# Optimization experiments

Hardware: AMD Instinct MI355X
Metric: run time of the kernel (lower is better)

The kernel has to match this reference:

```python
import jax, jax.numpy as jnp
import numpy as np

EPS = 1e-5
K = 16
DILATION = 1

def _bn(x, g, b, axes):
    # BatchNorm in training mode: batch statistics over all axes except channel (last)
    m = jnp.mean(x, axis=axes, keepdims=True)
    v = jnp.var(x, axis=axes, keepdims=True)
    return (x - m) * jax.lax.rsqrt(v + EPS) * g + b

def _knn_idx(p, q, k):
    # p: [B,N,3], q: [B,M,3] -> indices [B,M,k] of nearest points in p for each q
    d = (jnp.sum(q * q, -1)[:, :, None]
         - 2.0 * jnp.einsum('bmc,bnc->bmn', q, p)
         + jnp.sum(p * p, -1)[:, None, :])  # [B,M,N]
    _, idx = jax.lax.top_k(-d, k)
    return jax.lax.stop_gradient(idx)

def setup_inputs() -> dict:
    key = jax.random.key(0)
    ks = jax.random.split(key, 16)
    B, N, M, Cin, Cout = 8, 8192, 2048, 64, 128
    mid, K2 = Cout // 4, K * K
    s = 0.02
    d = {
        'p': jax.random.normal(ks[0], (B, N, 3), jnp.float32),
        'q': jax.random.normal(ks[1], (B, M, 3), jnp.float32),
        'x': jax.random.normal(ks[2], (B, Cin, N), jnp.float32),
        # mlp: two 1x1 convs (3->mid->mid) each with BN
        'W1': jax.random.normal(ks[3], (mid, 3), jnp.float32) * s,
        'b1': jnp.zeros((mid,), jnp.float32),
        'g1': jnp.ones((mid,), jnp.float32), 'be1': jnp.zeros((mid,), jnp.float32),
        'W2': jax.random.normal(ks[4], (mid, mid), jnp.float32) * s,
        'b2': jnp.zeros((mid,), jnp.float32),
        'g2': jnp.ones((mid,), jnp.float32), 'be2': jnp.zeros((mid,), jnp.float32),
        # stn: conv [1,K] (3->K^2), then two 1x1 convs (K^2->K^2)
        'Ws1': jax.random.normal(ks[5], (K2, 3, K), jnp.float32) * s,
        'bs1': jnp.zeros((K2,), jnp.float32),
        'gs1': jnp.ones((K2,), jnp.float32), 'bes1': jnp.zeros((K2,), jnp.float32),
        'Ws2': jax.random.normal(ks[6], (K2, K2), jnp.float32) * s,
        'bs2': jnp.zeros((K2,), jnp.float32),
        'gs2': jnp.ones((K2,), jnp.float32), 'bes2': jnp.zeros((K2,), jnp.float32),
        'Ws3': jax.random.normal(ks[7], (K2, K2), jnp.float32) * s,
        'bs3': jnp.zeros((K2,), jnp.float32),
        # final conv [1,K]: (Cin+mid -> Cout) with BN
        'Wc': jax.random.normal(ks[8], (Cout, Cin + mid, K), jnp.float32) * s,
        'bc': jnp.zeros((Cout,), jnp.float32),
        'gc': jnp.ones((Cout,), jnp.float32), 'bec': jnp.zeros((Cout,), jnp.float32),
    }
    return d

def reference(p, q, x, W1, b1, g1, be1, W2, b2, g2, be2,
              Ws1, bs1, gs1, bes1, Ws2, bs2, gs2, bes2, Ws3, bs3,
              Wc, bc, gc, bec):
    B, M = q.shape[0], q.shape[1]
    idx = _knn_idx(p, q, K * DILATION)[..., ::DILATION]  # [B,M,K]
    # gather neighbor coords and center: p_hat [B,M,K,3]
    p_n = jax.vmap(lambda a, i: a[i])(p, idx)
    p_hat = p_n - q[:, :, None, :]
    # mlp (pointwise convs, channel-last)
    h = jax.nn.relu(_bn(jnp.einsum('bmkc,oc->bmko', p_hat, W1) + b1, g1, be1, (0, 1, 2)))
    h = jax.nn.relu(_bn(jnp.einsum('bmkc,oc->bmko', h, W2) + b2, g2, be2, (0, 1, 2)))
    # gather features: x [B,Cin,N] -> [B,M,K,Cin]
    xt = jnp.transpose(x, (0, 2, 1))
    x_n = jax.vmap(lambda a, i: a[i])(xt, idx)
    x_hat = jnp.concatenate([h, x_n], axis=-1)  # [B,M,K,mid+Cin]
    # stn -> transform T [B,M,K,K]
    t = jax.nn.relu(_bn(jnp.einsum('bmkc,ock->bmo', p_hat, Ws1) + bs1, gs1, bes1, (0, 1)))
    t = jax.nn.relu(_bn(jnp.einsum('bmi,oi->bmo', t, Ws2) + bs2, gs2, bes2, (0, 1)))
    t = jnp.einsum('bmi,oi->bmo', t, Ws3) + bs3  # [B,M,K*K]
    T = t.reshape(B, M, K, K)
    x2 = jnp.einsum('bmij,bmjc->bmic', T, x_hat)  # [B,M,K,mid+Cin]
    out = jax.nn.relu(_bn(jnp.einsum('bmkc,ock->bmo', x2, Wc) + bc, gc, bec, (0, 1)))  # [B,M,Cout]
    return (q, jnp.transpose(out, (0, 2, 1)))  # q, x:[B,Cout,M]
```

## Files before the change

kernel.cpp:

```cpp
#include <hip/hip_runtime.h>
#include <hip/hip_bf16.h>


#define EPS 1e-5f

constexpr int Bb   = 8;
constexpr int Np   = 8192;
constexpr int Mq   = 2048;
constexpr int COUT = 128;
constexpr int BM   = Bb * Mq;
constexpr int BMK  = BM * 16;
constexpr int GC   = 16;
constexpr int NC   = GC * GC * GC;
constexpr int CAP  = 320;

typedef __attribute__((ext_vector_type(8))) short short8;
typedef __attribute__((ext_vector_type(4))) short short4v;
typedef __attribute__((ext_vector_type(4))) float f32x4;

__device__ __forceinline__ unsigned short f2bf(float x) {
  unsigned u = __float_as_uint(x);
  u += 0x7fffu + ((u >> 16) & 1u);
  return (unsigned short)(u >> 16);
}
__device__ __forceinline__ float bf2f_lo(unsigned v) { return __uint_as_float(v << 16); }
__device__ __forceinline__ float bf2f_hi(unsigned v) { return __uint_as_float(v & 0xffff0000u); }
__device__ __forceinline__ float bfround(float x) {
  return __uint_as_float(((unsigned)f2bf(x)) << 16);
}

__device__ __forceinline__ int cell_of(float c) {
  int v = (int)floorf(c * 2.0f + 8.0f);
  return v < 0 ? 0 : (v > 15 ? 15 : v);
}

__device__ __forceinline__ unsigned enc_dist(float d) {
  unsigned uu = __float_as_uint(d);
  return uu ^ (((unsigned)(((int)uu) >> 31)) | 0x80000000u);
}

__device__ __forceinline__ void bsort64(unsigned long long& v, int lane) {
#pragma unroll
  for (int k = 2; k <= 64; k <<= 1) {
#pragma unroll
    for (int jj = k >> 1; jj > 0; jj >>= 1) {
      unsigned long long o = __shfl_xor(v, jj);
      bool keepMin = (((lane & k) == 0) == ((lane & jj) == 0));
      unsigned long long mn = v < o ? v : o;
      unsigned long long mx = v < o ? o : v;
      v = keepMin ? mn : mx;
    }
  }
}
__device__ __forceinline__ void bmerge64(unsigned long long& v, int lane) {
#pragma unroll
  for (int jj = 32; jj > 0; jj >>= 1) {
    unsigned long long o = __shfl_xor(v, jj);
    bool keepMin = ((lane & jj) == 0);
    unsigned long long mn = v < o ? v : o;
    unsigned long long mx = v < o ? o : v;
    v = keepMin ? mn : mx;
  }
}
__device__ __forceinline__ unsigned long long sort_smallest64(const unsigned long long* buf,
                                                              int C, int lane) {
  unsigned long long run = (lane < C) ? buf[lane] : ~0ULL;
  bsort64(run, lane);
  for (int b2 = 64; b2 < C; b2 += 64) {
    unsigned long long v = (b2 + lane < C) ? buf[b2 + lane] : ~0ULL;
    bsort64(v, lane);
    unsigned long long vr = __shfl_xor(v, 63);
    unsigned long long m = run < vr ? run : vr;
    bmerge64(m, lane);
    run = m;
  }
  return run;
}


__device__ __forceinline__ void bn1_compute(int o, const float* __restrict__ st,
                                            const float* __restrict__ W1,
                                            const float* __restrict__ b1,
                                            const float* __restrict__ g1,
                                            const float* __restrict__ be1,
                                            float* sc_out, float* shf_out) {
  float n = (float)BMK;
  float w0 = W1[3 * o], w1 = W1[3 * o + 1], w2 = W1[3 * o + 2], b = b1[o];
  float s0 = st[0], s1 = st[1], s2 = st[2];
  float m00 = st[3], m11 = st[4], m22 = st[5], m01 = st[6], m02 = st[7], m12 = st[8];
  float ws = (w0 * s0 + w1 * s1 + w2 * s2) / n;
  float mean = b + ws;
  float quad = w0 * w0 * m00 + w1 * w1 * m11 + w2 * w2 * m22 +
               2.f * (w0 * w1 * m01 + w0 * w2 * m02 + w1 * w2 * m12);
  float ex2 = quad / n + 2.f * b * ws + b * b;
  float var = ex2 - mean * mean;
  float sc = g1[o] * rsqrtf(var + EPS);
  *sc_out = sc;
  *shf_out = be1[o] - mean * sc + b * sc;
}

__global__ __launch_bounds__(256) void prep_kernel(const float* __restrict__ p,
                                                   const float* __restrict__ x,
                                                   const float* __restrict__ Wc,
                                                   const float* __restrict__ Ws1,
                                                   float4* __restrict__ pp4,
                                                   float* __restrict__ xt,
                                                   unsigned short* __restrict__ wcrp,
                                                   unsigned short* __restrict__ ws1r,
                                                   int* __restrict__ hist) {
  __shared__ float tile[64][65];
  int blk = blockIdx.x;
  int tid = threadIdx.x;
  if (blk < 256) {
    int i = blk * 256 + tid;
    float px = p[3 * i], py = p[3 * i + 1], pz = p[3 * i + 2];
    float pp = __fadd_rn(__fadd_rn(__fmul_rn(px, px), __fmul_rn(py, py)), __fmul_rn(pz, pz));
    pp4[i] = make_float4(px, py, pz, pp);
    int b = i >> 13;
    int cid = (cell_of(px) << 8) | (cell_of(py) << 4) | cell_of(pz);
    atomicAdd(&hist[b * NC + cid], 1);
  } else if (blk < 1280) {
    int bx = blk - 256;
    int b = bx >> 7;
    int n0 = (bx & 127) << 6;
    int nl = tid & 63;
    int r0 = tid >> 6;
    const float* xb = x + (size_t)b * 64 * Np;
    for (int c = r0; c < 64; c += 4) tile[c][nl] = xb[(size_t)c * Np + n0 + nl];
    __syncthreads();
    float* xtb = xt + (size_t)b * Np * 64;
    for (int n = r0; n < 64; n += 4) xtb[(size_t)(n0 + n) * 64 + nl] = tile[nl][n];
  } else if (blk < 2048) {
    int g = (blk - 1280) * 256 + tid;
    if (g < 128 * 1536) {
      int o = g / 1536, r = g % 1536;
      int c = r % 96, j = r / 96;
      wcrp[g] = f2bf(Wc[(size_t)o * 1536 + c * 16 + j]);
    }
  } else {
    int g = (blk - 2048) * 256 + tid;
    int o = g >> 6, i = g & 63;
    float val = 0.f;
    if (i < 48) {
      int k = i / 3, c = i - 3 * k;
      val = Ws1[(size_t)o * 48 + c * 16 + k];
    }
    unsigned short h = f2bf(val);
    float hf = __uint_as_float(((unsigned)h) << 16);
    unsigned short l = f2bf(val - hf);
    ws1r[g] = h;
    ws1r[16384 + g] = l;
  }
}

__global__ __launch_bounds__(256) void prefix_kernel(const int* __restrict__ hist,
                                                     int* __restrict__ cellstart,
                                                     int* __restrict__ cursor) {
  __shared__ int ls[256];
  int b = blockIdx.x, t = threadIdx.x;
  const int* h = hist + b * NC;
  int loc[16], s = 0;
#pragma unroll
  for (int k = 0; k < 16; ++k) { loc[k] = h[t * 16 + k]; s += loc[k]; }
  ls[t] = s;
  __syncthreads();
  for (int off = 1; off < 256; off <<= 1) {
    int v = (t >= off) ? ls[t - off] : 0;
    __syncthreads();
    ls[t] += v;
    __syncthreads();
  }
  int run = ls[t] - s;
  int* cs = cellstart + b * (NC + 1);
  int* cu = cursor + b * NC;
#pragma unroll
  for (int k = 0; k < 16; ++k) {
    cs[t * 16 + k] = run;
    cu[t * 16 + k] = run;
    run += loc[k];
  }
  if (t == 255) cs[NC] = run;
}

__global__ __launch_bounds__(256) void scatter_kernel(const float4* __restrict__ pp4,
                                                      int* __restrict__ cursor,
                                                      float4* __restrict__ sp4,
                                                      int* __restrict__ sidx) {
  int i = blockIdx.x * 256 + threadIdx.x;
  int b = i >> 13;
  float4 pv = pp4[i];
  int cid = (cell_of(pv.x) << 8) | (cell_of(pv.y) << 4) | cell_of(pv.z);
  int pos = atomicAdd(&cursor[b * NC + cid], 1);
  sp4[(size_t)b * Np + pos] = pv;
  sidx[(size_t)b * Np + pos] = i & 8191;
}

__global__ __launch_bounds__(256) void knn_kernel(const float4* __restrict__ pp4,
                                                  const float4* __restrict__ sp4,
                                                  const int* __restrict__ sidx,
                                                  const int* __restrict__ cellstart,
                                                  const float* __restrict__ q,
                                                  int* __restrict__ idx_out) {
  __shared__ unsigned long long cand[4][CAP];
  int tid = threadIdx.x;
  int wslot = tid >> 6;
  int qi = blockIdx.x * 4 + wslot;
  int lane = tid & 63;
  int b = qi >> 11;
  const float4* pb = pp4 + (size_t)b * Np;
  const float4* sp = sp4 + (size_t)b * Np;
  const int* sx = sidx + (size_t)b * Np;
  const int* cs = cellstart + b * (NC + 1);
  const float* qp = q + (size_t)qi * 3;
  float qx = qp[0], qy = qp[1], qz = qp[2];
  float qqv = __fadd_rn(__fadd_rn(__fmul_rn(qx, qx), __fmul_rn(qy, qy)), __fmul_rn(qz, qz));
  float tau_f = INFINITY;

  {
    int cx = cell_of(qx), cy = cell_of(qy), cz = cell_of(qz);
    int alo = 0, blo = 0, nbw = 1, ncols = 1, zlo = 0, zhi = 0;
    int myS = 0, myE = 0;
    for (int r = 0;; ++r) {
      alo = cx - r; if (alo < 0) alo = 0;
      int ahi = cx + r; if (ahi > 15) ahi = 15;
      blo = cy - r; if (blo < 0) blo = 0;
      int bhi = cy + r; if (bhi > 15) bhi = 15;
      zlo = cz - r; if (zlo < 0) zlo = 0;
      zhi = cz + r; if (zhi > 15) zhi = 15;
      nbw = bhi - blo + 1;
      ncols = (ahi - alo + 1) * nbw;
      int total = 0;
      for (int l0 = 0; l0 < ncols; l0 += 64) {
        int l = l0 + lane;
        int sL = 0, eL = 0;
        if (l < ncols) {
          int da = l / nbw, db = l - da * nbw;
          int cbase = ((alo + da) << 8) | ((blo + db) << 4);
          sL = cs[cbase + zlo];
          eL = cs[cbase + zhi + 1];
        }
        if (l0 == 0) { myS = sL; myE = eL; }
        total += eL - sL;
      }
#pragma unroll
      for (int o = 32; o > 0; o >>= 1) total += __shfl_xor(total, o);
      if (total >= 16 || r >= 15) break;
    }
    unsigned u0 = 0xFFFFFFFFu, u1 = 0xFFFFFFFFu;
    int wcnt = 0;
    int ccen = (cx - alo) * nbw + (cy - blo);
    for (int c2 = 0; c2 < ncols && wcnt < 128; ++c2) {
      int cc = (c2 == 0) ? ccen : (c2 <= ccen ? c2 - 1 : c2);
      int s0, e;
      if (cc < 64) {
        s0 = __shfl(myS, cc);
        e = __shfl(myE, cc);
      } else {
        int da = cc / nbw, db = cc - da * nbw;
        int cbase = ((alo + da) << 8) | ((blo + db) << 4);
        s0 = cs[cbase + zlo];
        e = cs[cbase + zhi + 1];
      }
      for (int off = s0; off < e && wcnt < 128; off += 64) {
        int rem = e - off; if (rem > 64) rem = 64;
        int rot = wcnt & 63;
        int rel = (lane - rot) & 63;
        int g = wcnt + rel;
        if (rel < rem && g < 128) {
          float4 pv = sp[off + rel];
          float ee = __fmaf_rn(qz, pv.z, __fmaf_rn(qy, pv.y, __fmul_rn(qx, pv.x)));
          float d = __fadd_rn(__fsub_rn(qqv, __fmul_rn(2.0f, ee)), pv.w);
          unsigned uu = enc_dist(d);
          if (g < 64) u0 = uu; else u1 = uu;
        }
        wcnt += rem;
      }
    }
    unsigned lo = 0u, hi = 0xFF800000u;
    for (int it = 0; it < 20; ++it) {
      unsigned mid = lo + ((hi - lo) >> 1);
      int c = (int)__popcll(__ballot(u0 <= mid)) + (int)__popcll(__ballot(u1 <= mid));
      if (c >= 16) hi = mid; else lo = mid + 1;
    }
    tau_f = (hi >= 0x80000000u) ? __uint_as_float(hi ^ 0x80000000u)
                                : __uint_as_float(~hi);
  }

  int cnt = 0;
  unsigned long long lanebelow = (1ULL << lane) - 1ULL;
  {
    float R = sqrtf(fmaxf(tau_f, 0.f) + 3e-5f) * 1.0005f;
    int ax0 = cell_of(qx - R), ax1 = cell_of(qx + R);
    int ay0 = cell_of(qy - R), ay1 = cell_of(qy + R);
    int az0 = cell_of(qz - R), az1 = cell_of(qz + R);
    int nby = ay1 - ay0 + 1;
    int ncols = (ax1 - ax0 + 1) * nby;
    int myS = 0, myE = 0;
    if (lane < ncols) {
      int da = lane / nby, db = lane - da * nby;
      int cbase = ((ax0 + da) << 8) | ((ay0 + db) << 4);
      myS = cs[cbase + az0];
      myE = cs[cbase + az1 + 1];
    }
    for (int cc = 0; cc < ncols; ++cc) {
      int s0, e;
      if (cc < 64) {
        s0 = __shfl(myS, cc);
        e = __shfl(myE, cc);
      } else {
        int da = cc / nby, db = cc - da * nby;
        int cbase = ((ax0 + da) << 8) | ((ay0 + db) << 4);
        s0 = cs[cbase + az0];
        e = cs[cbase + az1 + 1];
      }
      for (int off = s0; off < e; off += 64) {
        int pos = off + lane;
        bool valid = pos < e;
        float4 pv = sp[valid ? pos : s0];
        float ee = __fmaf_rn(qz, pv.z, __fmaf_rn(qy, pv.y, __fmul_rn(qx, pv.x)));
        float d = __fadd_rn(__fsub_rn(qqv, __fmul_rn(2.0f, ee)), pv.w);
        if (!valid) d = __uint_as_float(0x7FC00000u);
        unsigned long long mask = __ballot(d <= tau_f);
        if (mask) {
          if (d <= tau_f) {
            int oi = sx[pos];
            unsigned uu = enc_dist(d);
            int wp = cnt + (int)__popcll(mask & lanebelow);
            if (wp < CAP)
              cand[wslot][wp] = (((unsigned long long)uu) << 32) | (unsigned)oi;
          }
          cnt += (int)__popcll(mask);
        }
      }
    }
  }
  __syncthreads();

  if (cnt <= CAP) {
    unsigned long long run = sort_smallest64(&cand[wslot][0], cnt, lane);
    if (lane < 16)
      idx_out[(size_t)qi * 16 + lane] = (int)(run & 0xffffffffULL);
  } else {
    unsigned long long kk = ~0ULL;
    float tl = tau_f;
    for (int base = 0; base < Np; base += 64) {
      float4 pv = pb[base + lane];
      float ee = __fmaf_rn(qz, pv.z, __fmaf_rn(qy, pv.y, __fmul_rn(qx, pv.x)));
      float dv = __fadd_rn(__fsub_rn(qqv, __fmul_rn(2.0f, ee)), pv.w);
      unsigned long long mask = __ballot(dv <= tl);
      if (mask) {
        unsigned uu = enc_dist(dv);
        unsigned long long cd = (((unsigned long long)uu) << 32) | (unsigned)(base + lane);
        do {
          int src = __ffsll((unsigned long long)mask) - 1;
          mask &= mask - 1;
          unsigned long long ck = __shfl(cd, src);
          unsigned long long up = __shfl_up(kk, 1);
          if (lane == 0) up = 0ULL;
          if (lane < 16 && ck < kk) kk = (up > ck) ? up : ck;
        } while (mask);
        unsigned long long tt = __shfl(kk, 15);
        unsigned tm = (unsigned)(tt >> 32);
        unsigned inv2 = tm ^ ((tm & 0x80000000u) ? 0x80000000u : 0xFFFFFFFFu);
        float tc = (tm == 0xFFFFFFFFu) ? INFINITY : __uint_as_float(inv2);
        if (tc < tl) tl = tc;
      }
    }
    if (lane < 16)
      idx_out[(size_t)qi * 16 + lane] = (int)(kk & 0xffffffffULL);
  }
}

__global__ __launch_bounds__(256) void phat_stats_kernel(const float4* __restrict__ pp4,
                                                         const float* __restrict__ q,
                                                         const int* __restrict__ idx,
                                                         float* __restrict__ phat,
                                                         float* __restrict__ stats) {
  float a[9];
#pragma unroll
  for (int k = 0; k < 9; ++k) a[k] = 0.f;
  int tid = threadIdx.x;
  for (int it = 0; it < 4; ++it) {
    int bmk = blockIdx.x * 256 + tid + it * 65536;
    int bm = bmk >> 4;
    int b = bm >> 11;
    int j = idx[bmk];
    float4 pv = pp4[(size_t)b * Np + j];
    const float* qp = q + (size_t)bm * 3;
    float h0 = pv.x - qp[0], h1 = pv.y - qp[1], h2 = pv.z - qp[2];
    phat[(size_t)bmk * 3 + 0] = h0;
    phat[(size_t)bmk * 3 + 1] = h1;
    phat[(size_t)bmk * 3 + 2] = h2;
    a[0] += h0; a[1] += h1; a[2] += h2;
    a[3] += h0 * h0; a[4] += h1 * h1; a[5] += h2 * h2;
    a[6] += h0 * h1; a[7] += h0 * h2; a[8] += h1 * h2;
  }
#pragma unroll
  for (int off = 32; off > 0; off >>= 1)
#pragma unroll
    for (int k = 0; k < 9; ++k) a[k] += __shfl_down(a[k], off);
  __shared__ float ls[9];
  if (tid < 9) ls[tid] = 0.f;
  __syncthreads();
  if ((tid & 63) == 0)
    for (int k = 0; k < 9; ++k) atomicAdd(&ls[k], a[k]);
  __syncthreads();
  if (tid < 9) atomicAdd(&stats[tid], ls[tid]);
}

__global__ __launch_bounds__(256) void stats2_kernel(const float* __restrict__ phat,
                                                     const float* __restrict__ stats,
                                                     const float* __restrict__ W1,
                                                     const float* __restrict__ b1,
                                                     const float* __restrict__ g1,
                                                     const float* __restrict__ be1,
                                                     const float* __restrict__ W2,
                                                     const float* __restrict__ b2,
                                                     float* __restrict__ stats2) {
  __shared__ float hsh[256 * 36];
  __shared__ float w2s[32 * 33];
  __shared__ float w1s[96], sc1[32], sh1[32], b2s[32], ls[64];
  int tid = threadIdx.x;
  if (tid < 32) {
    bn1_compute(tid, stats, W1, b1, g1, be1, &sc1[tid], &sh1[tid]);
    b2s[tid] = b2[tid];
  }
  if (tid < 96) w1s[tid] = W1[tid];
  if (tid < 64) ls[tid] = 0.f;
  for (int e = tid; e < 1024; e += 256) w2s[(e >> 5) * 33 + (e & 31)] = W2[e];
  __syncthreads();
  {
    int bmk = blockIdx.x * 256 + tid;
    float h0 = phat[(size_t)bmk * 3], hy = phat[(size_t)bmk * 3 + 1], hz = phat[(size_t)bmk * 3 + 2];
#pragma unroll
    for (int o4 = 0; o4 < 8; ++o4) {
      float4 r;
      float* rp = (float*)&r;
#pragma unroll
      for (int u = 0; u < 4; ++u) {
        int o = o4 * 4 + u;
        float t = w1s[3 * o] * h0 + w1s[3 * o + 1] * hy + w1s[3 * o + 2] * hz;
        rp[u] = fmaxf(0.f, t * sc1[o] + sh1[o]);
      }
      *(float4*)&hsh[tid * 36 + o4 * 4] = r;
    }
  }
  __syncthreads();
  int oc = tid & 31, grp = tid >> 5;
  float wrow[32];
#pragma unroll
  for (int c = 0; c < 32; ++c) wrow[c] = w2s[oc * 33 + c];
  float bias = b2s[oc];
  float ss = 0.f, qq = 0.f;
  for (int r = 0; r < 32; ++r) {
    int row = grp * 32 + r;
    float a = bias;
    const float4* hr = (const float4*)&hsh[row * 36];
#pragma unroll
    for (int c4 = 0; c4 < 8; ++c4) {
      float4 hv = hr[c4];
      a += hv.x * wrow[c4 * 4 + 0];
      a += hv.y * wrow[c4 * 4 + 1];
      a += hv.z * wrow[c4 * 4 + 2];
      a += hv.w * wrow[c4 * 4 + 3];
    }
    ss += a;
    qq += a * a;
  }
  atomicAdd(&ls[oc], ss);
  atomicAdd(&ls[32 + oc], qq);
  __syncthreads();
  if (tid < 64) atomicAdd(&stats2[tid], ls[tid]);
}

__global__ __launch_bounds__(256) void stn1_kernel(const float* __restrict__ phat,
                                                   const unsigned short* __restrict__ ws1r,
                                                   const float* __restrict__ bs1,
                                                   float* __restrict__ pt1,
                                                   float* __restrict__ spt1) {
  __shared__ unsigned short Ah[64 * 72], Al[64 * 72], Bh[128 * 72], Bl[128 * 72];
  __shared__ float ls[256];
  int tid = threadIdx.x;
  ls[tid] = 0.f;
  int mb = blockIdx.x >> 1, nb = blockIdx.x & 1;
  int bm0 = mb * 64, o0 = nb * 128;
  {
    int zr = tid >> 2, zc = 48 + (tid & 3) * 4;
    *(unsigned long long*)&Ah[zr * 72 + zc] = 0ULL;
    *(unsigned long long*)&Al[zr * 72 + zc] = 0ULL;
  }
  {
    int ar = tid >> 2, aseg = tid & 3;
    const float* Ap = phat + (size_t)(bm0 + ar) * 48 + aseg * 12;
    float4 v0 = *(const float4*)(Ap);
    float4 v1 = *(const float4*)(Ap + 4);
    float4 v2 = *(const float4*)(Ap + 8);
    float av[12] = {v0.x, v0.y, v0.z, v0.w, v1.x, v1.y, v1.z, v1.w, v2.x, v2.y, v2.z, v2.w};
    unsigned long long ph[3] = {0ULL, 0ULL, 0ULL}, pl[3] = {0ULL, 0ULL, 0ULL};
#pragma unroll
    for (int t = 0; t < 12; ++t) {
      unsigned short h = f2bf(av[t]);
      float hf = __uint_as_float(((unsigned)h) << 16);
      unsigned short l = f2bf(av[t] - hf);
      ph[t >> 2] |= ((unsigned long long)h) << ((t & 3) * 16);
      pl[t >> 2] |= ((unsigned long long)l) << ((t & 3) * 16);
    }
    int base = ar * 72 + aseg * 12;
#pragma unroll
    for (int t4 = 0; t4 < 3; ++t4) {
      *(unsigned long long*)&Ah[base + t4 * 4] = ph[t4];
      *(unsigned long long*)&Al[base + t4 * 4] = pl[t4];
    }
  }
#pragma unroll
  for (int pass = 0; pass < 4; ++pass) {
    int g = pass * 2048 + tid * 8;
    int br = g >> 6, i2 = g & 63;
    short8 vh = *(const short8*)&ws1r[(size_t)(o0 + br) * 64 + i2];
    short8 vl = *(const short8*)&ws1r[16384 + (size_t)(o0 + br) * 64 + i2];
    *(short8*)&Bh[br * 72 + i2] = vh;
    *(short8*)&Bl[br * 72 + i2] = vl;
  }
  __syncthreads();
  int wid = tid >> 6, lane = tid & 63;
  int wm = wid >> 1, wn = wid & 1;
  int mh = lane & 15, quad = lane >> 4;
  f32x4 acc[2][4];
#pragma unroll
  for (int a = 0; a < 2; ++a)
#pragma unroll
    for (int bq = 0; bq < 4; ++bq) acc[a][bq] = (f32x4){0.f, 0.f, 0.f, 0.f};
#pragma unroll
  for (int kc = 0; kc < 2; ++kc) {
    int ko = kc * 32 + quad * 8;
#pragma unroll
    for (int mt = 0; mt < 2; ++mt) {
      short8 ah = *(const short8*)&Ah[(wm * 32 + mt * 16 + mh) * 72 + ko];
      short8 al = *(const short8*)&Al[(wm * 32 + mt * 16 + mh) * 72 + ko];
#pragma unroll
      for (int nt = 0; nt < 4; ++nt) {
        short8 bh = *(const short8*)&Bh[(wn * 64 + nt * 16 + mh) * 72 + ko];
        short8 bl = *(const short8*)&Bl[(wn * 64 + nt * 16 + mh) * 72 + ko];
        acc[mt][nt] = __builtin_amdgcn_mfma_f32_16x16x32_bf16(ah, bh, acc[mt][nt], 0, 0, 0);
        acc[mt][nt] = __builtin_amdgcn_mfma_f32_16x16x32_bf16(ah, bl, acc[mt][nt], 0, 0, 0);
        acc[mt][nt] = __builtin_amdgcn_mfma_f32_16x16x32_bf16(al, bh, acc[mt][nt], 0, 0, 0);
      }
    }
  }
#pragma unroll
  for (int mt = 0; mt < 2; ++mt)
#pragma unroll
    for (int nt = 0; nt < 4; ++nt) {
      int colL = wn * 64 + nt * 16 + mh;
      int col = o0 + colL;
      float bvv = bs1[col];
      float ps = 0.f, pq = 0.f;
#pragma unroll
      for (int r = 0; r < 4; ++r) {
        float val = acc[mt][nt][r] + bvv;
        pt1[(size_t)(bm0 + wm * 32 + mt * 16 + quad * 4 + r) * 256 + col] = val;
        ps += val;
        pq += val * val;
      }
      atomicAdd(&ls[colL], ps);
      atomicAdd(&ls[128 + colL], pq);
    }
  __syncthreads();
  if (tid < 128) {
    atomicAdd(&spt1[o0 + tid], ls[tid]);
    atomicAdd(&spt1[256 + o0 + tid], ls[128 + tid]);
  }
}

__global__ __launch_bounds__(256) void stn_mm_kernel(const float* __restrict__ in,
                                                     const float* __restrict__ sums,
                                                     const float* __restrict__ gg,
                                                     const float* __restrict__ be,
                                                     const float* __restrict__ W,
                                                     const float* __restrict__ bias,
                                                     float* __restrict__ out,
                                                     float* __restrict__ outstats,
                                                     int do_stats) {
  __shared__ unsigned short As[64 * 40], Bs[128 * 40];
  __shared__ float scA[256], shA[256], ls[256];
  int tid = threadIdx.x;
  ls[tid] = 0.f;
  {
    float n = (float)BM;
    float mean = sums[tid] / n;
    float var = sums[256 + tid] / n - mean * mean;
    float s = gg[tid] * rsqrtf(var + EPS);
    scA[tid] = s;
    shA[tid] = be[tid] - mean * s;
  }
  int mb = blockIdx.x >> 1, nb = blockIdx.x & 1;
  int bm0 = mb * 64, o0 = nb * 128;
  int wid = tid >> 6, lane = tid & 63;
  int wm = wid >> 1, wn = wid & 1;
  int mh = lane & 15, quad = lane >> 4;
  f32x4 acc[2][4];
#pragma unroll
  for (int a = 0; a < 2; ++a)
#pragma unroll
    for (int bq = 0; bq < 4; ++bq) acc[a][bq] = (f32x4){0.f, 0.f, 0.f, 0.f};
  int ar = tid >> 2, aseg = tid & 3;
  const float* Ag = in + (size_t)(bm0 + ar) * 256 + aseg * 8;
  int aoff = ar * 40 + aseg * 8;
  int ci = aseg * 8;
  for (int i0 = 0; i0 < 256; i0 += 32) {
    __syncthreads();
    float4 v0 = *(const float4*)(Ag + i0);
    float4 v1 = *(const float4*)(Ag + i0 + 4);
    float av[8] = {v0.x, v0.y, v0.z, v0.w, v1.x, v1.y, v1.z, v1.w};
    short8 ap;
#pragma unroll
    for (int k = 0; k < 8; ++k)
      ap[k] = (short)f2bf(fmaxf(0.f, av[k] * scA[i0 + ci + k] + shA[i0 + ci + k]));
    *(short8*)&As[aoff] = ap;
#pragma unroll
    for (int jb = 0; jb < 2; ++jb) {
      int br = jb * 64 + ar;
      const float* Bg = W + (size_t)(o0 + br) * 256 + aseg * 8;
      float4 u0 = *(const float4*)(Bg + i0);
      float4 u1 = *(const float4*)(Bg + i0 + 4);
      float bv[8] = {u0.x, u0.y, u0.z, u0.w, u1.x, u1.y, u1.z, u1.w};
      short8 bp;
#pragma unroll
      for (int k = 0; k < 8; ++k) bp[k] = (short)f2bf(bv[k]);
      *(short8*)&Bs[br * 40 + aseg * 8] = bp;
    }
    __syncthreads();
#pragma unroll
    for (int mt = 0; mt < 2; ++mt) {
      short8 af = *(const short8*)&As[(wm * 32 + mt * 16 + mh) * 40 + quad * 8];
#pragma unroll
      for (int nt = 0; nt < 4; ++nt) {
        short8 bf = *(const short8*)&Bs[(wn * 64 + nt * 16 + mh) * 40 + quad * 8];
        acc[mt][nt] = __builtin_amdgcn_mfma_f32_16x16x32_bf16(af, bf, acc[mt][nt], 0, 0, 0);
      }
    }
  }
#pragma unroll
  for (int mt = 0; mt < 2; ++mt)
#pragma unroll
    for (int nt = 0; nt < 4; ++nt) {
      int colL = wn * 64 + nt * 16 + mh;
      int col = o0 + colL;
      float bvv = bias[col];
      float ps = 0.f, pq = 0.f;
#pragma unroll
      for (int r = 0; r < 4; ++r) {
        float val = acc[mt][nt][r] + bvv;
        out[(size_t)(bm0 + wm * 32 + mt * 16 + quad * 4 + r) * 256 + col] = val;
        ps += val;
        pq += val * val;
      }
      if (do_stats) {
        atomicAdd(&ls[colL], ps);
        atomicAdd(&ls[128 + colL], pq);
      }
    }
  if (do_stats) {
    __syncthreads();
    if (tid < 128) {
      atomicAdd(&outstats[o0 + tid], ls[tid]);
      atomicAdd(&outstats[256 + o0 + tid], ls[128 + tid]);
    }
  }
}

__global__ __launch_bounds__(256) void xhat_x2_kernel(const float* __restrict__ phat,
                                                      const float* __restrict__ stats,
                                                      const float* __restrict__ stats2,
                                                      const float* __restrict__ W1,
                                                      const float* __restrict__ b1,
                                                      const float* __restrict__ g1,
                                                      const float* __restrict__ be1,
                                                      const float* __restrict__ W2,
                                                      const float* __restrict__ b2,
                                                      const float* __restrict__ g2,
                                                      const float* __restrict__ be2,
                                                      const float* __restrict__ xt,
                                                      const int* __restrict__ idx,
                                                      const float* __restrict__ Tbuf,
                                                      unsigned short* __restrict__ x2) {
  __shared__ unsigned xh[256 * 17];
  __shared__ float Tst[256 * 16];
  __shared__ float sc1[32], sh1[32], sc2[32], sh2[32];
  int tid = threadIdx.x;
  if (tid < 32) {
    bn1_compute(tid, stats, W1, b1, g1, be1, &sc1[tid], &sh1[tid]);
    float n = (float)BMK;
    float mean = stats2[tid] / n;
    float var = stats2[32 + tid] / n - mean * mean;
    float s = g2[tid] * rsqrtf(var + EPS);
    sc2[tid] = s;
    sh2[tid] = be2[tid] - mean * s + b2[tid] * s;
  }
  __syncthreads();
  int bm0 = blockIdx.x * 16;
  int b = bm0 >> 11;
  int bml = tid >> 4, j = tid & 15;
  int bmk = (bm0 + bml) * 16 + j;
  {
    float h0 = phat[(size_t)bmk * 3], hy = phat[(size_t)bmk * 3 + 1], hz = phat[(size_t)bmk * 3 + 2];
    float h1v[32];
#pragma unroll
    for (int o = 0; o < 32; ++o) {
      float t = W1[3 * o] * h0 + W1[3 * o + 1] * hy + W1[3 * o + 2] * hz;
      h1v[o] = fmaxf(0.f, t * sc1[o] + sh1[o]);
    }
#pragma unroll
    for (int o4 = 0; o4 < 8; ++o4) {
      float r[4];
#pragma unroll
      for (int u = 0; u < 4; ++u) {
        int o = o4 * 4 + u;
        float a = 0.f;
#pragma unroll
        for (int c = 0; c < 32; ++c) a += h1v[c] * W2[o * 32 + c];
        r[u] = fmaxf(0.f, a * sc2[o] + sh2[o]);
      }
      xh[tid * 17 + o4 * 2] = (unsigned)f2bf(r[0]) | (((unsigned)f2bf(r[1])) << 16);
      xh[tid * 17 + o4 * 2 + 1] = (unsigned)f2bf(r[2]) | (((unsigned)f2bf(r[3])) << 16);
    }
    const float4* tg = (const float4*)(Tbuf + (size_t)(bm0 + bml) * 256 + j * 16);
    float4* td = (float4*)&Tst[tid * 16];
    td[0] = tg[0]; td[1] = tg[1]; td[2] = tg[2]; td[3] = tg[3];
  }
  __syncthreads();
  int cl = j;
  {
    float vlo[16], vhi[16];
#pragma unroll
    for (int jj = 0; jj < 16; ++jj) {
      unsigned uv = xh[(bml * 16 + jj) * 17 + cl];
      vlo[jj] = bf2f_lo(uv);
      vhi[jj] = bf2f_hi(uv);
    }
    for (int jo = 0; jo < 16; ++jo) {
      const float4* tr4 = (const float4*)&Tst[(bml * 16 + jo) * 16];
      float4 ta = tr4[0], tb = tr4[1], tc = tr4[2], tdd = tr4[3];
      float trow[16] = {ta.x, ta.y, ta.z, ta.w, tb.x, tb.y, tb.z, tb.w,
                        tc.x, tc.y, tc.z, tc.w, tdd.x, tdd.y, tdd.z, tdd.w};
      float a0 = 0.f, a1 = 0.f;
#pragma unroll
      for (int jj = 0; jj < 16; ++jj) {
        a0 += trow[jj] * vlo[jj];
        a1 += trow[jj] * vhi[jj];
      }
      unsigned* dst = (unsigned*)(x2 + (size_t)((bm0 + bml) * 16 + jo) * 96);
      dst[cl] = (unsigned)f2bf(a0) | (((unsigned)f2bf(a1)) << 16);
    }
  }
  {
    const int* idxrow = idx + (size_t)(bm0 + bml) * 16;
    float v0[16], v1[16], v2[16], v3[16];
#pragma unroll
    for (int jj = 0; jj < 16; ++jj) {
      int jx = idxrow[jj];
      float4 xv = *(const float4*)(xt + ((size_t)b * Np + jx) * 64 + cl * 4);
      v0[jj] = bfround(xv.x);
      v1[jj] = bfround(xv.y);
      v2[jj] = bfround(xv.z);
      v3[jj] = bfround(xv.w);
    }
    for (int jo = 0; jo < 16; ++jo) {
      const float4* tr4 = (const float4*)&Tst[(bml * 16 + jo) * 16];
      float4 ta = tr4[0], tb = tr4[1], tc = tr4[2], tdd = tr4[3];
      float trow[16] = {ta.x, ta.y, ta.z, ta.w, tb.x, tb.y, tb.z, tb.w,
                        tc.x, tc.y, tc.z, tc.w, tdd.x, tdd.y, tdd.z, tdd.w};
      float a0 = 0.f, a1 = 0.f, a2 = 0.f, a3 = 0.f;
#pragma unroll
      for (int jj = 0; jj < 16; ++jj) {
        float t = trow[jj];
        a0 += t * v0[jj];
        a1 += t * v1[jj];
        a2 += t * v2[jj];
        a3 += t * v3[jj];
      }
      unsigned* dst = (unsigned*)(x2 + (size_t)((bm0 + bml) * 16 + jo) * 96);
      dst[16 + cl * 2] = (unsigned)f2bf(a0) | (((unsigned)f2bf(a1)) << 16);
      dst[17 + cl * 2] = (unsigned)f2bf(a2) | (((unsigned)f2bf(a3)) << 16);
    }
  }
}

__global__ __launch_bounds__(256) void preout_kernel(const unsigned short* __restrict__ x2,
                                                     const unsigned short* __restrict__ Wcrp,
                                                     const float* __restrict__ bc,
                                                     float* __restrict__ pout,
                                                     float* __restrict__ spout) {
  __shared__ unsigned short As[32 * 40], Bs[128 * 40];
  __shared__ float ls[256];
  int tid = threadIdx.x;
  ls[tid] = 0.f;
  int bm0 = blockIdx.x * 32;
  int wid = tid >> 6, lane = tid & 63;
  int mh = lane & 15, quad = lane >> 4;
  f32x4 acc[2][2];
#pragma unroll
  for (int a = 0; a < 2; ++a)
#pragma unroll
    for (int bq = 0; bq < 2; ++bq) acc[a][bq] = (f32x4){0.f, 0.f, 0.f, 0.f};
  int ar = tid >> 3, aseg = tid & 7;
  int br = tid >> 1, bseg = tid & 1;
  const unsigned short* Ag = x2 + (size_t)(bm0 + ar) * 1536 + aseg * 4;
  const unsigned short* Bg = Wcrp + (size_t)br * 1536 + bseg * 16;
  int aoff = ar * 40 + aseg * 4;
  int boff = br * 40 + bseg * 16;
  short4v a_pre = *(const short4v*)Ag;
  short8 b_pre0 = *(const short8*)Bg;
  short8 b_pre1 = *(const short8*)(Bg + 8);
  for (int i0 = 0; i0 < 1536; i0 += 32) {
    __syncthreads();
    *(short4v*)&As[aoff] = a_pre;
    *(short8*)&Bs[boff] = b_pre0;
    *(short8*)&Bs[boff + 8] = b_pre1;
    __syncthreads();
    if (i0 + 32 < 1536) {
      a_pre = *(const short4v*)(Ag + i0 + 32);
      b_pre0 = *(const short8*)(Bg + i0 + 32);
      b_pre1 = *(const short8*)(Bg + i0 + 40);
    }
#pragma unroll
    for (int mt = 0; mt < 2; ++mt) {
      short8 af = *(const short8*)&As[(mt * 16 + mh) * 40 + quad * 8];
#pragma unroll
      for (int nt = 0; nt < 2; ++nt) {
        short8 bf = *(const short8*)&Bs[(wid * 32 + nt * 16 + mh) * 40 + quad * 8];
        acc[mt][nt] = __builtin_amdgcn_mfma_f32_16x16x32_bf16(af, bf, acc[mt][nt], 0, 0, 0);
      }
    }
  }
#pragma unroll
  for (int mt = 0; mt < 2; ++mt)
#pragma unroll
    for (int nt = 0; nt < 2; ++nt) {
      int col = wid * 32 + nt * 16 + mh;
      float bvv = bc[col];
      float ps = 0.f, pq = 0.f;
#pragma unroll
      for (int r = 0; r < 4; ++r) {
        float val = acc[mt][nt][r] + bvv;
        pout[(size_t)(bm0 + mt * 16 + quad * 4 + r) * 128 + col] = val;
        ps += val;
        pq += val * val;
      }
      atomicAdd(&ls[col], ps);
      atomicAdd(&ls[128 + col], pq);
    }
  __syncthreads();
  atomicAdd(&spout[tid], ls[tid]);
}

__global__ __launch_bounds__(256) void final_kernel(const float* __restrict__ q,
                                                    const float* __restrict__ pout,
                                                    const float* __restrict__ scs,
                                                    const float* __restrict__ gc,
                                                    const float* __restrict__ bec,
                                                    float* __restrict__ dout) {
  __shared__ float ldsT[128 * 65];
  int blk = blockIdx.x;
  int tid = threadIdx.x;
  if (blk < 192) {
    int g = blk * 256 + tid;
    dout[g] = q[g];
    return;
  }
  int blk2 = blk - 192;
  int b = blk2 >> 5;
  int m0 = (blk2 & 31) * 64;
  int row = tid >> 2, seg = tid & 3;
  const float4* src = (const float4*)(pout + ((size_t)(b * Mq) + m0 + row) * 128 + seg * 32);
#pragma unroll
  for (int k4 = 0; k4 < 8; ++k4) {
    float4 v = src[k4];
    int o = seg * 32 + k4 * 4;
    ldsT[(o + 0) * 65 + row] = v.x;
    ldsT[(o + 1) * 65 + row] = v.y;
    ldsT[(o + 2) * 65 + row] = v.z;
    ldsT[(o + 3) * 65 + row] = v.w;
  }
  __syncthreads();
  int lane = tid & 63, wv = tid >> 6;
  float n = (float)BM;
  float* base = dout + (size_t)BM * 3 + (size_t)b * COUT * Mq + m0;
#pragma unroll
  for (int rep = 0; rep < 32; ++rep) {
    int o = wv * 32 + rep;
    float mean = scs[o] / n;
    float var = scs[128 + o] / n - mean * mean;
    float s = gc[o] * rsqrtf(var + EPS);
    float shv = bec[o] - mean * s;
    float v = ldsT[o * 65 + lane];
    base[(size_t)o * Mq + lane] = fmaxf(0.f, v * s + shv);
  }
}

extern "C" void kernel_launch(void* const* d_in, const int* in_sizes, int n_in, void* d_out,
                              int out_size, void* d_ws, size_t ws_size, hipStream_t stream) {
  const float* p = (const float*)d_in[0];
  const float* q = (const float*)d_in[1];
  const float* x = (const float*)d_in[2];
  const float* W1 = (const float*)d_in[3];
  const float* b1 = (const float*)d_in[4];
  const float* g1 = (const float*)d_in[5];
  const float* be1 = (const float*)d_in[6];
  const float* W2 = (const float*)d_in[7];
  const float* b2 = (const float*)d_in[8];
  const float* g2 = (const float*)d_in[9];
  const float* be2 = (const float*)d_in[10];
  const float* Ws1 = (const float*)d_in[11];
  const float* bs1 = (const float*)d_in[12];
  const float* gs1 = (const float*)d_in[13];
  const float* bes1 = (const float*)d_in[14];
  const float* Ws2 = (const float*)d_in[15];
  const float* bs2 = (const float*)d_in[16];
  const float* gs2 = (const float*)d_in[17];
  const float* bes2 = (const float*)d_in[18];
  const float* Ws3 = (const float*)d_in[19];
  const float* bs3 = (const float*)d_in[20];
  const float* Wc = (const float*)d_in[21];
  const float* bc = (const float*)d_in[22];
  const float* gc = (const float*)d_in[23];
  const float* bec = (const float*)d_in[24];
  float* dout = (float*)d_out;

  char* ws = (char*)d_ws;
  float* stats = (float*)ws;
  size_t off = 8192;
  float4* pp4 = (float4*)(ws + off);  off += (size_t)Bb * Np * 16;
  int* idxb = (int*)(ws + off);       off += (size_t)BMK * 4;
  float* xt = (float*)(ws + off);     off += (size_t)Bb * Np * 64 * 4;
  float* phat = (float*)(ws + off);   off += (size_t)BMK * 3 * 4;
  float* pt1 = (float*)(ws + off);    off += (size_t)BM * 256 * 4;
  float* pt2 = (float*)(ws + off);    off += (size_t)BM * 256 * 4;
  float* Tb = (float*)(ws + off);     off += (size_t)BM * 256 * 4;
  float* pout = (float*)(ws + off);   off += (size_t)BM * 128 * 4;
  unsigned short* wcrp = (unsigned short*)(ws + off); off += (size_t)1536 * 128 * 2;
  unsigned short* x2 = (unsigned short*)(ws + off);   off += (size_t)BM * 1536 * 2;
  int* hist = (int*)(ws + off);       off += (size_t)Bb * NC * 4;
  int* cursor = (int*)(ws + off);     off += (size_t)Bb * NC * 4;
  int* cellstart = (int*)(ws + off);  off += (size_t)Bb * (NC + 1) * 4;
  float4* sp4 = (float4*)(ws + off);  off += (size_t)Bb * Np * 16;
  int* sidx = (int*)(ws + off);       off += (size_t)Bb * Np * 4;
  unsigned short* ws1r = (unsigned short*)(ws + off); off += (size_t)2 * 256 * 64 * 2;

  hipMemsetAsync(stats, 0, 8192, stream);
  hipMemsetAsync(hist, 0, (size_t)Bb * NC * 4, stream);
  hipLaunchKernelGGL(prep_kernel, dim3(2112), dim3(256), 0, stream, p, x, Wc, Ws1, pp4, xt, wcrp, ws1r, hist);
  hipLaunchKernelGGL(prefix_kernel, dim3(8), dim3(256), 0, stream, hist, cellstart, cursor);
  hipLaunchKernelGGL(scatter_kernel, dim3(256), dim3(256), 0, stream, pp4, cursor, sp4, sidx);
  hipLaunchKernelGGL(knn_kernel, dim3(4096), dim3(256), 0, stream, pp4, sp4, sidx, cellstart, q, idxb);
  hipLaunchKernelGGL(phat_stats_kernel, dim3(256), dim3(256), 0, stream, pp4, q, idxb, phat, stats);
  hipLaunchKernelGGL(stn1_kernel, dim3(512), dim3(256), 0, stream, phat, ws1r, bs1, pt1, stats + 128);
  hipLaunchKernelGGL(stats2_kernel, dim3(1024), dim3(256), 0, stream, phat, stats, W1, b1, g1, be1, W2, b2, stats + 16);
  hipLaunchKernelGGL(stn_mm_kernel, dim3(512), dim3(256), 0, stream, pt1, stats + 128, gs1, bes1, Ws2, bs2, pt2, stats + 640, 1);
  hipLaunchKernelGGL(stn_mm_kernel, dim3(512), dim3(256), 0, stream, pt2, stats + 640, gs2, bes2, Ws3, bs3, Tb, (float*)nullptr, 0);
  hipLaunchKernelGGL(xhat_x2_kernel, dim3(1024), dim3(256), 0, stream, phat, stats, stats + 16,
                     W1, b1, g1, be1, W2, b2, g2, be2, xt, idxb, Tb, x2);
  hipLaunchKernelGGL(preout_kernel, dim3(512), dim3(256), 0, stream, x2, wcrp, bc, pout, stats + 1152);
  hipLaunchKernelGGL(final_kernel, dim3(448), dim3(256), 0, stream, q, pout, stats + 1152, gc, bec, dout);
}
```

Measured before the change: 364.8 us.

## Enlarge preout GEMM tile to 64 rows, pad T smem, hoist idx loads

The preout GEMM block tile grows from 32 to 64 rows, with a 2x2 warp layout (32x64 per warp) and 8-element vector loads for both operands. This halves the grid and the number of times the weight matrix is reloaded per output row. The xhat_x2 kernel pads the shared T rows to a stride of 20 floats to cut bank conflicts, and loads the neighbour indices early so their latency overlaps the MLP compute. In exchange, each thread keeps more accumulator registers, and the smaller grid may reduce occupancy.

```diff
diff --git a/kernel.cpp b/kernel.cpp
--- a/kernel.cpp
+++ b/kernel.cpp
@@ -13,9 +13,9 @@
 constexpr int GC   = 16;
 constexpr int NC   = GC * GC * GC;
 constexpr int CAP  = 320;
+constexpr int TS   = 20;
 
 typedef __attribute__((ext_vector_type(8))) short short8;
-typedef __attribute__((ext_vector_type(4))) short short4v;
 typedef __attribute__((ext_vector_type(4))) float f32x4;
 
 __device__ __forceinline__ unsigned short f2bf(float x) {
@@ -685,7 +685,7 @@
                                                       const float* __restrict__ Tbuf,
                                                       unsigned short* __restrict__ x2) {
   __shared__ unsigned xh[256 * 17];
-  __shared__ float Tst[256 * 16];
+  __shared__ float Tst[256 * TS];
   __shared__ float sc1[32], sh1[32], sc2[32], sh2[32];
   int tid = threadIdx.x;
   if (tid < 32) {
@@ -702,6 +702,12 @@
   int b = bm0 >> 11;
   int bml = tid >> 4, j = tid & 15;
   int bmk = (bm0 + bml) * 16 + j;
+  int jxr[16];
+  {
+    const int* idxrow = idx + (size_t)(bm0 + bml) * 16;
+#pragma unroll
+    for (int jj = 0; jj < 16; ++jj) jxr[jj] = idxrow[jj];
+  }
   {
     float h0 = phat[(size_t)bmk * 3], hy = phat[(size_t)bmk * 3 + 1], hz = phat[(size_t)bmk * 3 + 2];
     float h1v[32];
@@ -725,7 +731,7 @@
       xh[tid * 17 + o4 * 2 + 1] = (unsigned)f2bf(r[2]) | (((unsigned)f2bf(r[3])) << 16);
     }
     const float4* tg = (const float4*)(Tbuf + (size_t)(bm0 + bml) * 256 + j * 16);
-    float4* td = (float4*)&Tst[tid * 16];
+    float4* td = (float4*)&Tst[tid * TS];
     td[0] = tg[0]; td[1] = tg[1]; td[2] = tg[2]; td[3] = tg[3];
   }
   __syncthreads();
@@ -739,7 +745,7 @@
       vhi[jj] = bf2f_hi(uv);
     }
     for (int jo = 0; jo < 16; ++jo) {
-      const float4* tr4 = (const float4*)&Tst[(bml * 16 + jo) * 16];
+      const float4* tr4 = (const float4*)&Tst[(bml * 16 + jo) * TS];
       float4 ta = tr4[0], tb = tr4[1], tc = tr4[2], tdd = tr4[3];
       float trow[16] = {ta.x, ta.y, ta.z, ta.w, tb.x, tb.y, tb.z, tb.w,
                         tc.x, tc.y, tc.z, tc.w, tdd.x, tdd.y, tdd.z, tdd.w};
@@ -754,11 +760,10 @@
     }
   }
   {
-    const int* idxrow = idx + (size_t)(bm0 + bml) * 16;
     float v0[16], v1[16], v2[16], v3[16];
 #pragma unroll
     for (int jj = 0; jj < 16; ++jj) {
-      int jx = idxrow[jj];
+      int jx = jxr[jj];
       float4 xv = *(const float4*)(xt + ((size_t)b * Np + jx) * 64 + cl * 4);
       v0[jj] = bfround(xv.x);
       v1[jj] = bfround(xv.y);
@@ -766,7 +771,7 @@
       v3[jj] = bfround(xv.w);
     }
     for (int jo = 0; jo < 16; ++jo) {
-      const float4* tr4 = (const float4*)&Tst[(bml * 16 + jo) * 16];
+      const float4* tr4 = (const float4*)&Tst[(bml * 16 + jo) * TS];
       float4 ta = tr4[0], tb = tr4[1], tc = tr4[2], tdd = tr4[3];
       float trow[16] = {ta.x, ta.y, ta.z, ta.w, tb.x, tb.y, tb.z, tb.w,
                         tc.x, tc.y, tc.z, tc.w, tdd.x, tdd.y, tdd.z, tdd.w};
@@ -791,44 +796,44 @@
                                                      const float* __restrict__ bc,
                                                      float* __restrict__ pout,
                                                      float* __restrict__ spout) {
-  __shared__ unsigned short As[32 * 40], Bs[128 * 40];
+  __shared__ unsigned short As[64 * 40], Bs[128 * 40];
   __shared__ float ls[256];
   int tid = threadIdx.x;
   ls[tid] = 0.f;
-  int bm0 = blockIdx.x * 32;
+  int bm0 = blockIdx.x * 64;
   int wid = tid >> 6, lane = tid & 63;
+  int wm = wid >> 1, wn = wid & 1;
   int mh = lane & 15, quad = lane >> 4;
-  f32x4 acc[2][2];
+  f32x4 acc[2][4];
 #pragma unroll
   for (int a = 0; a < 2; ++a)
 #pragma unroll
-    for (int bq = 0; bq < 2; ++bq) acc[a][bq] = (f32x4){0.f, 0.f, 0.f, 0.f};
-  int ar = tid >> 3, aseg = tid & 7;
-  int br = tid >> 1, bseg = tid & 1;
-  const unsigned short* Ag = x2 + (size_t)(bm0 + ar) * 1536 + aseg * 4;
-  const unsigned short* Bg = Wcrp + (size_t)br * 1536 + bseg * 16;
-  int aoff = ar * 40 + aseg * 4;
-  int boff = br * 40 + bseg * 16;
-  short4v a_pre = *(const short4v*)Ag;
-  short8 b_pre0 = *(const short8*)Bg;
-  short8 b_pre1 = *(const short8*)(Bg + 8);
+    for (int bq = 0; bq < 4; ++bq) acc[a][bq] = (f32x4){0.f, 0.f, 0.f, 0.f};
+  int ar = tid >> 2, aseg = tid & 3;
+  const unsigned short* Ag = x2 + (size_t)(bm0 + ar) * 1536 + aseg * 8;
+  const unsigned short* Bg0 = Wcrp + (size_t)ar * 1536 + aseg * 8;
+  const unsigned short* Bg1 = Wcrp + (size_t)(64 + ar) * 1536 + aseg * 8;
+  int aoff = ar * 40 + aseg * 8;
+  short8 a_pre = *(const short8*)Ag;
+  short8 b_pre0 = *(const short8*)Bg0;
+  short8 b_pre1 = *(const short8*)Bg1;
   for (int i0 = 0; i0 < 1536; i0 += 32) {
     __syncthreads();
-    *(short4v*)&As[aoff] = a_pre;
-    *(short8*)&Bs[boff] = b_pre0;
-    *(short8*)&Bs[boff + 8] = b_pre1;
+    *(short8*)&As[aoff] = a_pre;
+    *(short8*)&Bs[aoff] = b_pre0;
+    *(short8*)&Bs[64 * 40 + aoff] = b_pre1;
     __syncthreads();
     if (i0 + 32 < 1536) {
-      a_pre = *(const short4v*)(Ag + i0 + 32);
-      b_pre0 = *(const short8*)(Bg + i0 + 32);
-      b_pre1 = *(const short8*)(Bg + i0 + 40);
+      a_pre = *(const short8*)(Ag + i0 + 32);
+      b_pre0 = *(const short8*)(Bg0 + i0 + 32);
+      b_pre1 = *(const short8*)(Bg1 + i0 + 32);
     }
 #pragma unroll
     for (int mt = 0; mt < 2; ++mt) {
-      short8 af = *(const short8*)&As[(mt * 16 + mh) * 40 + quad * 8];
-#pragma unroll
-      for (int nt = 0; nt < 2; ++nt) {
-        short8 bf = *(const short8*)&Bs[(wid * 32 + nt * 16 + mh) * 40 + quad * 8];
+      short8 af = *(const short8*)&As[(wm * 32 + mt * 16 + mh) * 40 + quad * 8];
+#pragma unroll
+      for (int nt = 0; nt < 4; ++nt) {
+        short8 bf = *(const short8*)&Bs[(wn * 64 + nt * 16 + mh) * 40 + quad * 8];
         acc[mt][nt] = __builtin_amdgcn_mfma_f32_16x16x32_bf16(af, bf, acc[mt][nt], 0, 0, 0);
       }
     }
@@ -836,14 +841,14 @@
 #pragma unroll
   for (int mt = 0; mt < 2; ++mt)
 #pragma unroll
-    for (int nt = 0; nt < 2; ++nt) {
-      int col = wid * 32 + nt * 16 + mh;
+    for (int nt = 0; nt < 4; ++nt) {
+      int col = wn * 64 + nt * 16 + mh;
       float bvv = bc[col];
       float ps = 0.f, pq = 0.f;
 #pragma unroll
       for (int r = 0; r < 4; ++r) {
         float val = acc[mt][nt][r] + bvv;
-        pout[(size_t)(bm0 + mt * 16 + quad * 4 + r) * 128 + col] = val;
+        pout[(size_t)(bm0 + wm * 32 + mt * 16 + quad * 4 + r) * 128 + col] = val;
         ps += val;
         pq += val * val;
       }
@@ -960,6 +965,6 @@
   hipLaunchKernelGGL(stn_mm_kernel, dim3(512), dim3(256), 0, stream, pt2, stats + 640, gs2, bes2, Ws3, bs3, Tb, (float*)nullptr, 0);
   hipLaunchKernelGGL(xhat_x2_kernel, dim3(1024), dim3(256), 0, stream, phat, stats, stats + 16,
                      W1, b1, g1, be1, W2, b2, g2, be2, xt, idxb, Tb, x2);
-  hipLaunchKernelGGL(preout_kernel, dim3(512), dim3(256), 0, stream, x2, wcrp, bc, pout, stats + 1152);
+  hipLaunchKernelGGL(preout_kernel, dim3(256), dim3(256), 0, stream, x2, wcrp, bc, pout, stats + 1152);
   hipLaunchKernelGGL(final_kernel, dim3(448), dim3(256), 0, stream, q, pout, stats + 1152, gc, bec, dout);
 }
```

Result: faster. 355.7 us (-2.5%).
